# Kernel optimization log

Measured on AMD Instinct MI355X. Metric: run time of the kernel, lower is better.

## Reference

```python
import jax, jax.numpy as jnp
import numpy as np

POS_W = 1.0
ANG_W = 1.0
WID_W = 1.0
N = 1048560  # predictions (divisible by 17)
M = 8388480  # total GT grasps = sum(arange(N) % 17)


def setup_inputs() -> dict:
    key = jax.random.key(0)
    k1, k2 = jax.random.split(key)
    pred = jax.random.normal(k1, (N, 6), dtype=jnp.float32)
    all_targets = jax.random.normal(k2, (M, 6), dtype=jnp.float32)
    # ragged counts in [0, 16]; sum == M exactly
    target_counts = (jnp.arange(N, dtype=jnp.int64) % 17)
    return {"pred": pred, "all_targets": all_targets, "target_counts": target_counts}


def _smooth_l1(x):
    a = jnp.abs(x)
    return jnp.where(a < 1.0, 0.5 * x * x, a - 0.5)


def reference(pred, all_targets, target_counts):
    n = pred.shape[0]
    m = all_targets.shape[0]
    # segment id for each GT row (contiguous slices, order of target_counts)
    seg = jnp.repeat(jnp.arange(n), target_counts, total_repeat_length=m)  # (M,)
    p = pred[seg]  # (M,6) gathered predictions
    dp = p[:, :2] - all_targets[:, :2]
    da = p[:, 2:4] - all_targets[:, 2:4]
    dw = p[:, 4] - all_targets[:, 4]
    dist = (POS_W * jnp.sum(dp * dp, axis=-1)
            + ANG_W * jnp.sum(da * da, axis=-1)
            + WID_W * dw * dw)  # (M,)
    # ragged argmin per segment (first occurrence, like torch.argmin)
    min_d = jax.ops.segment_min(dist, seg, num_segments=n)  # (N,)
    row = jnp.arange(m)
    cand = jnp.where(dist == min_d[seg], row, m)
    arg = jax.ops.segment_min(cand, seg, num_segments=n)  # (N,) global row idx or m
    has = target_counts > 0
    gt = all_targets[jnp.where(has, jnp.clip(arg, 0, m - 1), 0)]  # (N,6)
    # fused per-prediction loss against the closest GT
    loss_pos = jnp.sum(_smooth_l1(pred[:, :2] - gt[:, :2]), axis=-1)
    loss_ang = jnp.sum(jnp.abs(pred[:, 2:4] - gt[:, 2:4]), axis=-1)
    loss_wid = _smooth_l1(pred[:, 4] - gt[:, 4])
    losses = jnp.where(has, POS_W * loss_pos + ANG_W * loss_ang + WID_W * loss_wid, 0.0)
    return jnp.mean(losses)  # reduction='mean'
```

## Files before the change

kernel.cpp:

```cpp
#include <hip/hip_runtime.h>
#include <math.h>

#define POS_W 1.0f
#define ANG_W 1.0f
#define WID_W 1.0f
#define CHUNK 1024
#define F2PT 12

__device__ __forceinline__ float smooth_l1(float x) {
    float a = fabsf(x);
    return a < 1.0f ? 0.5f * x * x : a - 0.5f;
}

__global__ void k_block_sums(const int* __restrict__ counts, int stride, int n,
                             int* __restrict__ blockSums) {
    int i = blockIdx.x * 256 + threadIdx.x;
    int c = (i < n) ? counts[(long long)i * stride] : 0;
    for (int off = 32; off > 0; off >>= 1) c += __shfl_down(c, off, 64);
    __shared__ int sdata[4];
    int lane = threadIdx.x & 63, wave = threadIdx.x >> 6;
    if (lane == 0) sdata[wave] = c;
    __syncthreads();
    if (threadIdx.x == 0)
        blockSums[blockIdx.x] = sdata[0] + sdata[1] + sdata[2] + sdata[3];
}

__global__ void k_scan_blocks(const int* __restrict__ blockSums, int nb,
                              int* __restrict__ blockOffs) {
    int t = threadIdx.x;
    int per = (nb + 255) / 256;
    int start = t * per;
    int end = min(start + per, nb);
    int sum = 0;
    for (int j = start; j < end; ++j) sum += blockSums[j];
    __shared__ int s[256];
    s[t] = sum;
    __syncthreads();
    for (int d = 1; d < 256; d <<= 1) {
        int v = (t >= d) ? s[t - d] : 0;
        __syncthreads();
        s[t] += v;
        __syncthreads();
    }
    int run = s[t] - sum;
    for (int j = start; j < end; ++j) {
        blockOffs[j] = run;
        run += blockSums[j];
    }
}

__global__ __launch_bounds__(256) void k_loss(
    const float* __restrict__ pred, const float* __restrict__ tgt,
    const int* __restrict__ counts, int stride, int n,
    const int* __restrict__ blockOffs, float* __restrict__ partials) {
    __shared__ float2 ch[CHUNK * 3];
    __shared__ int wsum[4];
    __shared__ float fs[4];

    int t = threadIdx.x;
    int lane = t & 63, wave = t >> 6;
    int i = blockIdx.x * 256 + t;
    int c = (i < n) ? counts[(long long)i * stride] : 0;

    int incl = c;
#pragma unroll
    for (int d = 1; d < 64; d <<= 1) {
        int v = __shfl_up(incl, d, 64);
        if (lane >= d) incl += v;
    }
    if (lane == 63) wsum[wave] = incl;
    __syncthreads();
    int w0 = wsum[0], w1 = wsum[1], w2 = wsum[2], w3 = wsum[3];
    int waveOff = (wave > 0 ? w0 : 0) + (wave > 1 ? w1 : 0) + (wave > 2 ? w2 : 0);
    int off = waveOff + incl - c;
    int total = w0 + w1 + w2 + w3;
    int winStart = blockOffs[blockIdx.x];

    bool active = (i < n) && (c > 0);
    float p0 = 0, p1 = 0, p2 = 0, p3 = 0, p4 = 0;
    if (active) {
        const float2* p2p = (const float2*)(pred + (long long)i * 6);
        float2 a = p2p[0], b = p2p[1], w = p2p[2];
        p0 = a.x; p1 = a.y; p2 = b.x; p3 = b.y; p4 = w.x;
    }

    float best = INFINITY;
    float b0 = 0, b1 = 0, b2 = 0, b3 = 0, b4 = 0;

    const float2* win = (const float2*)tgt + (long long)winStart * 3;
    float2 r[F2PT];

    {
        int nF2 = min(CHUNK, total) * 3;
#pragma unroll
        for (int j = 0; j < F2PT; ++j) {
            int k = t + 256 * j;
            if (k < nF2) r[j] = win[k];
        }
    }

    for (int base = 0; base < total; base += CHUNK) {
        int rows = min(CHUNK, total - base);
        int nF2c = rows * 3;
#pragma unroll
        for (int j = 0; j < F2PT; ++j) {
            int k = t + 256 * j;
            if (k < nF2c) ch[k] = r[j];
        }
        __syncthreads();
        int nbase = base + CHUNK;
        if (nbase < total) {
            int nF2n = min(CHUNK, total - nbase) * 3;
            const float2* srcn = win + (long long)nbase * 3;
#pragma unroll
            for (int j = 0; j < F2PT; ++j) {
                int k = t + 256 * j;
                if (k < nF2n) r[j] = srcn[k];
            }
        }
        if (active) {
            int lo = max(off, base), hi = min(off + c, base + rows);
            for (int rr = lo; rr < hi; ++rr) {
                int l3 = (rr - base) * 3;
                float2 ga = ch[l3], gb = ch[l3 + 1], gw = ch[l3 + 2];
                float d0 = p0 - ga.x, d1 = p1 - ga.y;
                float d2 = p2 - gb.x, d3 = p3 - gb.y;
                float d4 = p4 - gw.x;
                float dist = POS_W * (d0 * d0 + d1 * d1) +
                             ANG_W * (d2 * d2 + d3 * d3) + WID_W * d4 * d4;
                if (dist < best) {
                    best = dist;
                    b0 = ga.x; b1 = ga.y; b2 = gb.x; b3 = gb.y; b4 = gw.x;
                }
            }
        }
        __syncthreads();
    }

    float loss = 0.0f;
    if (active) {
        loss = POS_W * (smooth_l1(p0 - b0) + smooth_l1(p1 - b1)) +
               ANG_W * (fabsf(p2 - b2) + fabsf(p3 - b3)) +
               WID_W * smooth_l1(p4 - b4);
    }

    for (int o = 32; o > 0; o >>= 1) loss += __shfl_down(loss, o, 64);
    if (lane == 0) fs[wave] = loss;
    __syncthreads();
    if (t == 0) partials[blockIdx.x] = fs[0] + fs[1] + fs[2] + fs[3];
}

__global__ void k_reduce(const float* __restrict__ partials, int nb,
                         float invN, float* __restrict__ out) {
    int t = threadIdx.x;
    float s = 0.0f;
    for (int j = t; j < nb; j += 256) s += partials[j];
    for (int o = 32; o > 0; o >>= 1) s += __shfl_down(s, o, 64);
    __shared__ float fs[4];
    int lane = t & 63, wave = t >> 6;
    if (lane == 0) fs[wave] = s;
    __syncthreads();
    if (t == 0) out[0] = (fs[0] + fs[1] + fs[2] + fs[3]) * invN;
}

extern "C" void kernel_launch(void* const* d_in, const int* in_sizes, int n_in,
                              void* d_out, int out_size, void* d_ws,
                              size_t ws_size, hipStream_t stream) {
    const float* pred = (const float*)d_in[0];
    const float* tgt = (const float*)d_in[1];
    const int* counts = (const int*)d_in[2];
    int n = in_sizes[0] / 6;
    int stride = (in_sizes[2] == n) ? 1 : 2;
    int nb = (n + 255) / 256;

    int* blockSums = (int*)d_ws;
    int* blockOffs = blockSums + nb;
    float* partials = (float*)(blockOffs + nb);
    float* out = (float*)d_out;

    k_block_sums<<<nb, 256, 0, stream>>>(counts, stride, n, blockSums);
    k_scan_blocks<<<1, 256, 0, stream>>>(blockSums, nb, blockOffs);
    k_loss<<<nb, 256, 0, stream>>>(pred, tgt, counts, stride, n, blockOffs,
                                   partials);
    k_reduce<<<1, 256, 0, stream>>>(partials, nb, 1.0f / n, out);
}
```

Measured before the change: 312.3 us.

## Parallelize ragged argmin over GT rows with LDS binary search and atomicMin

Replaces the per-prediction serial scan over its ragged GT segment with one thread per GT row. Each thread binary-searches the block's segment offsets in LDS to find its owning prediction, computes the distance, and does a 64-bit LDS atomicMin on a packed key of distance bits and local row index, so ties resolve to the first occurrence. The owning thread then reloads the winning target row from global memory to compute the loss. This removes intra-wave load imbalance from variable segment lengths and the chunked LDS staging. In exchange it adds a binary search, LDS atomics and an extra global gather per prediction.

```diff
diff --git a/kernel.cpp b/kernel.cpp
--- a/kernel.cpp
+++ b/kernel.cpp
@@ -4,8 +4,6 @@
 #define POS_W 1.0f
 #define ANG_W 1.0f
 #define WID_W 1.0f
-#define CHUNK 1024
-#define F2PT 12
 
 __device__ __forceinline__ float smooth_l1(float x) {
     float a = fabsf(x);
@@ -53,7 +51,9 @@
     const float* __restrict__ pred, const float* __restrict__ tgt,
     const int* __restrict__ counts, int stride, int n,
     const int* __restrict__ blockOffs, float* __restrict__ partials) {
-    __shared__ float2 ch[CHUNK * 3];
+    __shared__ int offs[257];
+    __shared__ float P0[256], P1[256], P2[256], P3[256], P4[256];
+    __shared__ unsigned long long mk[256];
     __shared__ int wsum[4];
     __shared__ float fs[4];
 
@@ -72,76 +72,59 @@
     __syncthreads();
     int w0 = wsum[0], w1 = wsum[1], w2 = wsum[2], w3 = wsum[3];
     int waveOff = (wave > 0 ? w0 : 0) + (wave > 1 ? w1 : 0) + (wave > 2 ? w2 : 0);
-    int off = waveOff + incl - c;
+    int myoff = waveOff + incl - c;
     int total = w0 + w1 + w2 + w3;
     int winStart = blockOffs[blockIdx.x];
 
     bool active = (i < n) && (c > 0);
     float p0 = 0, p1 = 0, p2 = 0, p3 = 0, p4 = 0;
-    if (active) {
+    if (i < n) {
         const float2* p2p = (const float2*)(pred + (long long)i * 6);
         float2 a = p2p[0], b = p2p[1], w = p2p[2];
         p0 = a.x; p1 = a.y; p2 = b.x; p3 = b.y; p4 = w.x;
     }
+    offs[t] = myoff;
+    if (t == 255) offs[256] = total;
+    P0[t] = p0; P1[t] = p1; P2[t] = p2; P3[t] = p3; P4[t] = p4;
+    mk[t] = ~0ULL;
+    __syncthreads();
 
-    float best = INFINITY;
-    float b0 = 0, b1 = 0, b2 = 0, b3 = 0, b4 = 0;
-
-    const float2* win = (const float2*)tgt + (long long)winStart * 3;
-    float2 r[F2PT];
-
-    {
-        int nF2 = min(CHUNK, total) * 3;
+    const float2* winp = (const float2*)tgt + (long long)winStart * 3;
+    for (int base = 0; base < total; base += 256) {
+        int rloc = base + t;
+        bool v = rloc < total;
+        float2 a, b, w;
+        const float2* rp = winp + (long long)rloc * 3;
+        if (v) { a = rp[0]; b = rp[1]; w = rp[2]; }
+        if (v) {
+            int lo = 0, hi = 256;
 #pragma unroll
-        for (int j = 0; j < F2PT; ++j) {
-            int k = t + 256 * j;
-            if (k < nF2) r[j] = win[k];
+            for (int s8 = 0; s8 < 8; ++s8) {
+                int mid = (lo + hi) >> 1;
+                if (offs[mid] <= rloc) lo = mid; else hi = mid;
+            }
+            int o = lo;
+            float d0 = P0[o] - a.x, d1 = P1[o] - a.y;
+            float d2 = P2[o] - b.x, d3 = P3[o] - b.y;
+            float d4 = P4[o] - w.x;
+            float dist = POS_W * (d0 * d0 + d1 * d1) +
+                         ANG_W * (d2 * d2 + d3 * d3) + WID_W * d4 * d4;
+            unsigned long long key =
+                ((unsigned long long)__float_as_uint(dist) << 21) |
+                (unsigned int)rloc;
+            atomicMin(&mk[o], key);
         }
     }
-
-    for (int base = 0; base < total; base += CHUNK) {
-        int rows = min(CHUNK, total - base);
-        int nF2c = rows * 3;
-#pragma unroll
-        for (int j = 0; j < F2PT; ++j) {
-            int k = t + 256 * j;
-            if (k < nF2c) ch[k] = r[j];
-        }
-        __syncthreads();
-        int nbase = base + CHUNK;
-        if (nbase < total) {
-            int nF2n = min(CHUNK, total - nbase) * 3;
-            const float2* srcn = win + (long long)nbase * 3;
-#pragma unroll
-            for (int j = 0; j < F2PT; ++j) {
-                int k = t + 256 * j;
-                if (k < nF2n) r[j] = srcn[k];
-            }
-        }
-        if (active) {
-            int lo = max(off, base), hi = min(off + c, base + rows);
-            for (int rr = lo; rr < hi; ++rr) {
-                int l3 = (rr - base) * 3;
-                float2 ga = ch[l3], gb = ch[l3 + 1], gw = ch[l3 + 2];
-                float d0 = p0 - ga.x, d1 = p1 - ga.y;
-                float d2 = p2 - gb.x, d3 = p3 - gb.y;
-                float d4 = p4 - gw.x;
-                float dist = POS_W * (d0 * d0 + d1 * d1) +
-                             ANG_W * (d2 * d2 + d3 * d3) + WID_W * d4 * d4;
-                if (dist < best) {
-                    best = dist;
-                    b0 = ga.x; b1 = ga.y; b2 = gb.x; b3 = gb.y; b4 = gw.x;
-                }
-            }
-        }
-        __syncthreads();
-    }
+    __syncthreads();
 
     float loss = 0.0f;
     if (active) {
-        loss = POS_W * (smooth_l1(p0 - b0) + smooth_l1(p1 - b1)) +
-               ANG_W * (fabsf(p2 - b2) + fabsf(p3 - b3)) +
-               WID_W * smooth_l1(p4 - b4);
+        int rloc = (int)(mk[t] & 0x1FFFFFULL);
+        const float2* rp = winp + (long long)rloc * 3;
+        float2 a = rp[0], b = rp[1], w = rp[2];
+        loss = POS_W * (smooth_l1(p0 - a.x) + smooth_l1(p1 - a.y)) +
+               ANG_W * (fabsf(p2 - b.x) + fabsf(p3 - b.y)) +
+               WID_W * smooth_l1(p4 - w.x);
     }
 
     for (int o = 32; o > 0; o >>= 1) loss += __shfl_down(loss, o, 64);
```

New measurement: 315.5 us. About the same (+1.0%).

## Stage targets per wavefront with double-buffered LDS and wave-local barriers

Applied to the files above, without the earlier changes.

Each wavefront now loads and stages only its own contiguous slice of target rows into a private double-buffered LDS region, synchronising with wave barriers instead of block-wide __syncthreads. Per-wave loss partials go straight to global memory, which removes the final block reduction, and the reduce kernel sums four times as many partials. The aim is to let the four waves of a block progress independently instead of stalling on each other in the chunked scan. In exchange, loads are clamped per lane and loop counts differ per wave, so load imbalance between waves remains.

```diff
diff --git a/kernel.cpp b/kernel.cpp
--- a/kernel.cpp
+++ b/kernel.cpp
@@ -4,8 +4,6 @@
 #define POS_W 1.0f
 #define ANG_W 1.0f
 #define WID_W 1.0f
-#define CHUNK 1024
-#define F2PT 12
 
 __device__ __forceinline__ float smooth_l1(float x) {
     float a = fabsf(x);
@@ -53,9 +51,8 @@
     const float* __restrict__ pred, const float* __restrict__ tgt,
     const int* __restrict__ counts, int stride, int n,
     const int* __restrict__ blockOffs, float* __restrict__ partials) {
-    __shared__ float2 ch[CHUNK * 3];
+    __shared__ float2 buf[4][2][768];
     __shared__ int wsum[4];
-    __shared__ float fs[4];
 
     int t = threadIdx.x;
     int lane = t & 63, wave = t >> 6;
@@ -70,15 +67,16 @@
     }
     if (lane == 63) wsum[wave] = incl;
     __syncthreads();
-    int w0 = wsum[0], w1 = wsum[1], w2 = wsum[2], w3 = wsum[3];
+    int w0 = wsum[0], w1 = wsum[1], w2 = wsum[2];
     int waveOff = (wave > 0 ? w0 : 0) + (wave > 1 ? w1 : 0) + (wave > 2 ? w2 : 0);
-    int off = waveOff + incl - c;
-    int total = w0 + w1 + w2 + w3;
-    int winStart = blockOffs[blockIdx.x];
+    int offW = incl - c;
+    int totalW = wsum[wave];
+    const float2* win = (const float2*)tgt +
+                        (long long)(blockOffs[blockIdx.x] + waveOff) * 3;
 
     bool active = (i < n) && (c > 0);
     float p0 = 0, p1 = 0, p2 = 0, p3 = 0, p4 = 0;
-    if (active) {
+    if (i < n) {
         const float2* p2p = (const float2*)(pred + (long long)i * 6);
         float2 a = p2p[0], b = p2p[1], w = p2p[2];
         p0 = a.x; p1 = a.y; p2 = b.x; p3 = b.y; p4 = w.x;
@@ -87,42 +85,32 @@
     float best = INFINITY;
     float b0 = 0, b1 = 0, b2 = 0, b3 = 0, b4 = 0;
 
-    const float2* win = (const float2*)tgt + (long long)winStart * 3;
-    float2 r[F2PT];
+    if (totalW > 0) {
+        int totalF2 = totalW * 3;
+        float2 r[12];
+        float2(*mybuf)[768] = buf[wave];
+#pragma unroll
+        for (int j = 0; j < 12; ++j)
+            r[j] = win[min(lane + 64 * j, totalF2 - 1)];
 
-    {
-        int nF2 = min(CHUNK, total) * 3;
+        int nch = (totalW + 255) >> 8;
+        for (int ck = 0; ck < nch; ++ck) {
+            float2* bb = mybuf[ck & 1];
 #pragma unroll
-        for (int j = 0; j < F2PT; ++j) {
-            int k = t + 256 * j;
-            if (k < nF2) r[j] = win[k];
-        }
-    }
-
-    for (int base = 0; base < total; base += CHUNK) {
-        int rows = min(CHUNK, total - base);
-        int nF2c = rows * 3;
+            for (int j = 0; j < 12; ++j) bb[lane + 64 * j] = r[j];
+            if (ck + 1 < nch) {
+                int kb = (ck + 1) * 768 + lane;
 #pragma unroll
-        for (int j = 0; j < F2PT; ++j) {
-            int k = t + 256 * j;
-            if (k < nF2c) ch[k] = r[j];
-        }
-        __syncthreads();
-        int nbase = base + CHUNK;
-        if (nbase < total) {
-            int nF2n = min(CHUNK, total - nbase) * 3;
-            const float2* srcn = win + (long long)nbase * 3;
-#pragma unroll
-            for (int j = 0; j < F2PT; ++j) {
-                int k = t + 256 * j;
-                if (k < nF2n) r[j] = srcn[k];
+                for (int j = 0; j < 12; ++j)
+                    r[j] = win[min(kb + 64 * j, totalF2 - 1)];
             }
-        }
-        if (active) {
-            int lo = max(off, base), hi = min(off + c, base + rows);
+            asm volatile("s_waitcnt lgkmcnt(0)" ::: "memory");
+            __builtin_amdgcn_wave_barrier();
+            int base = ck << 8;
+            int lo = max(offW, base), hi = min(offW + c, base + 256);
             for (int rr = lo; rr < hi; ++rr) {
                 int l3 = (rr - base) * 3;
-                float2 ga = ch[l3], gb = ch[l3 + 1], gw = ch[l3 + 2];
+                float2 ga = bb[l3], gb = bb[l3 + 1], gw = bb[l3 + 2];
                 float d0 = p0 - ga.x, d1 = p1 - ga.y;
                 float d2 = p2 - gb.x, d3 = p3 - gb.y;
                 float d4 = p4 - gw.x;
@@ -133,8 +121,8 @@
                     b0 = ga.x; b1 = ga.y; b2 = gb.x; b3 = gb.y; b4 = gw.x;
                 }
             }
+            __builtin_amdgcn_wave_barrier();
         }
-        __syncthreads();
     }
 
     float loss = 0.0f;
@@ -143,18 +131,15 @@
                ANG_W * (fabsf(p2 - b2) + fabsf(p3 - b3)) +
                WID_W * smooth_l1(p4 - b4);
     }
-
     for (int o = 32; o > 0; o >>= 1) loss += __shfl_down(loss, o, 64);
-    if (lane == 0) fs[wave] = loss;
-    __syncthreads();
-    if (t == 0) partials[blockIdx.x] = fs[0] + fs[1] + fs[2] + fs[3];
+    if (lane == 0) partials[blockIdx.x * 4 + wave] = loss;
 }
 
-__global__ void k_reduce(const float* __restrict__ partials, int nb,
+__global__ void k_reduce(const float* __restrict__ partials, int np,
                          float invN, float* __restrict__ out) {
     int t = threadIdx.x;
     float s = 0.0f;
-    for (int j = t; j < nb; j += 256) s += partials[j];
+    for (int j = t; j < np; j += 256) s += partials[j];
     for (int o = 32; o > 0; o >>= 1) s += __shfl_down(s, o, 64);
     __shared__ float fs[4];
     int lane = t & 63, wave = t >> 6;
@@ -182,5 +167,5 @@
     k_scan_blocks<<<1, 256, 0, stream>>>(blockSums, nb, blockOffs);
     k_loss<<<nb, 256, 0, stream>>>(pred, tgt, counts, stride, n, blockOffs,
                                    partials);
-    k_reduce<<<1, 256, 0, stream>>>(partials, nb, 1.0f / n, out);
+    k_reduce<<<1, 256, 0, stream>>>(partials, 4 * nb, 1.0f / n, out);
 }
```

Result: slower. 321.5 us (+3.0%).
